# Optimization experiments

Measured on AMD Instinct MI355X. Metric: run time of the kernel, lower is better.

Reference implementation:

```python
import jax, jax.numpy as jnp
import numpy as np

B, N, D, H, K = 8, 256, 128, 128, 8


def _kaiming_uniform(key, shape, fan_in):
    bound = np.sqrt(6.0 / fan_in)
    return jax.random.uniform(key, shape, jnp.float32, -bound, bound)


def setup_inputs() -> dict:
    key = jax.random.key(0)
    ks = jax.random.split(key, 5)
    E = jax.random.normal(ks[0], (B, N, D), jnp.float32)
    W1 = _kaiming_uniform(ks[1], (K, 2 * D, H), 2 * D)   # FFN2 layer 1
    b1 = jnp.zeros((K, H), jnp.float32)
    W2 = _kaiming_uniform(ks[2], (K, H, 2), H)           # FFN2 layer 2
    b2 = jnp.zeros((K, 2), jnp.float32)
    W3 = _kaiming_uniform(ks[3], (K, 2, 1), 2)           # FFN3
    b3 = jnp.zeros((K, 1), jnp.float32)
    return {"E": E, "W1": W1, "b1": b1, "W2": W2, "b2": b2, "W3": W3, "b3": b3}


def _entmax15_pair(logits):
    # Exact alpha=1.5 entmax over a last dim of size 2 (closed form).
    # z' = z/2; p_i = [z'_i - tau]_+^2 with sum(p)=1.
    t = (logits[..., 0] - logits[..., 1]) * 0.25   # signed half-gap of z'
    d = jnp.abs(t)
    s = jnp.sqrt(jnp.maximum(0.5 - d * d, 0.0))
    p0_interior = (s + t) ** 2                      # both coords in support
    p0 = jnp.where(d >= 0.5, (t > 0).astype(logits.dtype), p0_interior)
    return jnp.stack([p0, 1.0 - p0], axis=-1)


def reference(E, W1, b1, W2, b2, W3, b3):
    # E: [B,N,D]. Concat([Ei,Ej]) @ W1 == Ei @ W1[:D] + Ej @ W1[D:], so we never
    # materialize the [B,N,N,2D] pair tensor.
    Dd = E.shape[-1]
    W1i, W1j = W1[:, :Dd, :], W1[:, Dd:, :]
    outs = []
    for h in range(W1.shape[0]):  # small fixed head loop (k_basis)
        hi = jnp.einsum('bnd,dh->bnh', E, W1i[h])
        hj = jnp.einsum('bnd,dh->bnh', E, W1j[h])
        pre = hi[:, :, None, :] + hj[:, None, :, :] + b1[h]      # [B,N,N,H]
        act = jax.nn.relu(pre)                                    # dropout: eval mode (identity)
        logits2 = jnp.einsum('bijh,hc->bijc', act, W2[h]) + b2[h]  # [B,N,N,2]
        p2 = _entmax15_pair(logits2)
        a = jnp.einsum('bijc,co->bijo', p2, W3[h])[..., 0] + b3[h][0]  # [B,N,N]
        outs.append(a)
    M = jnp.stack(outs, axis=1)  # [B,K,N,N]
    n = E.shape[1]
    eye = jnp.eye(n, dtype=M.dtype)
    M = M * (1.0 - eye)[None, None]  # no_self_loop=True
    return M
```

## Files before the change

kernel.cpp:

```cpp
#include <hip/hip_runtime.h>
#include <hip/hip_fp16.h>
#include <cstdint>
#include <cstddef>

#define B_ 8
#define N_ 256
#define D_ 128
#define H_ 128
#define K_ 8

typedef _Float16 f16x8 __attribute__((ext_vector_type(8)));
typedef _Float16 f16x2 __attribute__((ext_vector_type(2)));
typedef float    f32x4 __attribute__((ext_vector_type(4)));

static __device__ __forceinline__ f16x2 h2cast(unsigned u) {
    return __builtin_bit_cast(f16x2, u);
}
static __device__ __forceinline__ unsigned packh2(float lo, float hi) {
    unsigned a = __half_as_ushort(__float2half(lo));
    unsigned b = __half_as_ushort(__float2half(hi));
    return a | (b << 16);
}

__global__ void prep_small(const float* __restrict__ W2, const float* __restrict__ b2,
                           const float* __restrict__ W3, const float* __restrict__ b3,
                           unsigned* __restrict__ wdh, float* __restrict__ consts) {
    int t = threadIdx.x;
    for (int idx = t; idx < K_ * 64; idx += 256) {
        int base = idx * 2;
        float w0 = W2[base * 2]     - W2[base * 2 + 1];
        float w1 = W2[base * 2 + 2] - W2[base * 2 + 3];
        wdh[idx] = packh2(w0, w1);
    }
    if (t < K_) {
        consts[t * 4 + 0] = b2[t * 2] - b2[t * 2 + 1];
        consts[t * 4 + 1] = W3[t * 2] - W3[t * 2 + 1];
        consts[t * 4 + 2] = W3[t * 2 + 1] + b3[t];
    }
}

__global__ __launch_bounds__(256) void prep_eh(const float* __restrict__ E,
                                               __half* __restrict__ Eh) {
    int idx = (blockIdx.x * 256 + threadIdx.x) * 4;
    float4 v = *(const float4*)&E[idx];
    uint2 o;
    o.x = packh2(v.x, v.y);
    o.y = packh2(v.z, v.w);
    *(uint2*)&Eh[idx] = o;
}

__global__ __launch_bounds__(256) void prep_wh(const float* __restrict__ W1,
                                               __half* __restrict__ Wh) {
    __shared__ float Ws[128][33];
    const int bid = blockIdx.x;
    const int ct  = bid & 7;
    const int k   = bid >> 3;
    const int c0  = ct * 32;
    const int ro  = (c0 < 128) ? 0 : 128;
    const int h0  = c0 & 127;
    const int t   = threadIdx.x;

    #pragma unroll
    for (int rep = 0; rep < 16; rep++) {
        int idx = rep * 256 + t;
        int d   = idx >> 5;
        int cl  = idx & 31;
        Ws[d][cl] = W1[((size_t)(k * 256 + ro + d)) * H_ + h0 + cl];
    }
    __syncthreads();

    const int cl = t >> 3;
    const int dg = t & 7;
    __half tmp[16];
    #pragma unroll
    for (int e = 0; e < 16; e++) tmp[e] = __float2half(Ws[dg * 16 + e][cl]);
    *(float4*)&Wh[((size_t)(k * 256 + c0 + cl)) * D_ + dg * 16]     = *(float4*)&tmp[0];
    *(float4*)&Wh[((size_t)(k * 256 + c0 + cl)) * D_ + dg * 16 + 8] = *(float4*)&tmp[8];
}

__global__ __launch_bounds__(256) void stage1_kernel(
        const __half* __restrict__ Eh, const __half* __restrict__ Wh,
        const float* __restrict__ b1, __half* __restrict__ Gh) {
    __shared__ __half Es[64 * 136];
    __shared__ __half Ws[64 * 136];

    const int bid = blockIdx.x;
    const int ct  = bid & 3;
    const int it  = (bid >> 2) & 3;
    const int bk  = bid >> 4;
    const int k   = bk & (K_ - 1);
    const int b   = bk >> 3;
    const int i0  = it * 64, c0 = ct * 64;
    const int t   = threadIdx.x;

    #pragma unroll
    for (int rep = 0; rep < 4; rep++) {
        int idx = rep * 256 + t;
        int r = idx >> 4;
        int q = idx & 15;
        *(float4*)&Es[r * 136 + q * 8] =
            *(const float4*)&Eh[((size_t)(b * N_ + i0 + r)) * D_ + q * 8];
        *(float4*)&Ws[r * 136 + q * 8] =
            *(const float4*)&Wh[((size_t)(k * 256 + c0 + r)) * D_ + q * 8];
    }
    __syncthreads();

    const int wv   = t >> 6;
    const int lane = t & 63;
    const int wr   = wv >> 1, wc = wv & 1;
    const int lr   = lane & 15, lk = lane >> 4;

    f32x4 acc[2][2] = {{{0.f,0.f,0.f,0.f},{0.f,0.f,0.f,0.f}},
                       {{0.f,0.f,0.f,0.f},{0.f,0.f,0.f,0.f}}};
    #pragma unroll
    for (int kk = 0; kk < 4; kk++) {
        f16x8 A[2], Bv[2];
        #pragma unroll
        for (int mi = 0; mi < 2; mi++)
            A[mi] = *(const f16x8*)&Es[(wr * 32 + mi * 16 + lr) * 136 + kk * 32 + lk * 8];
        #pragma unroll
        for (int ni = 0; ni < 2; ni++)
            Bv[ni] = *(const f16x8*)&Ws[(wc * 32 + ni * 16 + lr) * 136 + kk * 32 + lk * 8];
        #pragma unroll
        for (int mi = 0; mi < 2; mi++)
            #pragma unroll
            for (int ni = 0; ni < 2; ni++)
                acc[mi][ni] = __builtin_amdgcn_mfma_f32_16x16x32_f16(
                    A[mi], Bv[ni], acc[mi][ni], 0, 0, 0);
    }

    #pragma unroll
    for (int ni = 0; ni < 2; ni++) {
        int col = c0 + wc * 32 + ni * 16 + lr;
        float bias = (col < 128) ? b1[k * H_ + col] : 0.f;
        #pragma unroll
        for (int mi = 0; mi < 2; mi++) {
            int rbase = i0 + wr * 32 + mi * 16 + lk * 4;
            #pragma unroll
            for (int r = 0; r < 4; r++) {
                Gh[((size_t)(bk * N_ + rbase + r)) * 256 + col] =
                    __float2half(acc[mi][ni][r] + bias);
            }
        }
    }
}

__global__ __launch_bounds__(256) void stage2_kernel(
        const __half* __restrict__ Gh, const unsigned* __restrict__ wdh,
        const float* __restrict__ consts, float* __restrict__ out) {
    __shared__ __half his[64 * 136];
    __shared__ __half hjs[64 * 136];

    const int bid = blockIdx.x;
    const int jt  = bid & 3;
    const int it  = (bid >> 2) & 3;
    const int bk  = bid >> 4;
    const int k   = bk & (K_ - 1);
    const int i0  = it * 64, j0 = jt * 64;
    const int t   = threadIdx.x;

    const __half* __restrict__ gb = Gh + (size_t)bk * N_ * 256;

    #pragma unroll
    for (int rep = 0; rep < 4; rep++) {
        int idx = rep * 256 + t;
        int r = idx >> 4;
        int q = idx & 15;
        *(float4*)&his[r * 136 + q * 8] =
            *(const float4*)&gb[(size_t)(i0 + r) * 256 + q * 8];
        *(float4*)&hjs[r * 136 + q * 8] =
            *(const float4*)&gb[(size_t)(j0 + r) * 256 + 128 + q * 8];
    }
    __syncthreads();

    const float b2d = consts[k * 4 + 0];
    const float w3d = consts[k * 4 + 1];
    const float w3b = consts[k * 4 + 2];
    const int tx = t & 15;
    const int ty = t >> 4;

    float acc[4][4];
    #pragma unroll
    for (int a = 0; a < 4; a++)
        #pragma unroll
        for (int c = 0; c < 4; c++) acc[a][c] = b2d;

    const unsigned* __restrict__ wp = wdh + k * 64;
    const f16x2 zz = {(_Float16)0, (_Float16)0};

    #pragma unroll 2
    for (int hq = 0; hq < 16; hq++) {
        unsigned Wv[4];
        *(uint4*)&Wv[0] = *(const uint4*)&wp[hq * 4];
        unsigned Aa[4][4], Bb[4][4];
        #pragma unroll
        for (int a = 0; a < 4; a++)
            *(uint4*)&Aa[a][0] = *(const uint4*)&his[(ty + 16 * a) * 136 + hq * 8];
        #pragma unroll
        for (int c = 0; c < 4; c++)
            *(uint4*)&Bb[c][0] = *(const uint4*)&hjs[(tx + 16 * c) * 136 + hq * 8];

        #pragma unroll
        for (int e = 0; e < 4; e++) {
            f16x2 w2 = h2cast(Wv[e]);
            #pragma unroll
            for (int a = 0; a < 4; a++) {
                f16x2 av = h2cast(Aa[a][e]);
                #pragma unroll
                for (int c = 0; c < 4; c++) {
                    f16x2 pre = av + h2cast(Bb[c][e]);
                    f16x2 act = __builtin_elementwise_max(pre, zz);
                    acc[a][c] = __builtin_amdgcn_fdot2(act, w2, acc[a][c], false);
                }
            }
        }
    }

    #pragma unroll
    for (int a = 0; a < 4; a++) {
        int i = i0 + ty + 16 * a;
        #pragma unroll
        for (int c = 0; c < 4; c++) {
            float av = acc[a][c];
            float tt = av * 0.25f;
            float dd = fabsf(tt);
            float ss = sqrtf(fmaxf(0.5f - dd * dd, 0.f));
            float p0i = (ss + tt) * (ss + tt);
            float p0 = (dd >= 0.5f) ? (tt > 0.f ? 1.f : 0.f) : p0i;
            float val = fmaf(p0, w3d, w3b);
            int j = j0 + tx + 16 * c;
            if (i == j) val = 0.f;
            out[((size_t)bk * N_ + i) * N_ + j] = val;
        }
    }
}

extern "C" void kernel_launch(void* const* d_in, const int* in_sizes, int n_in,
                              void* d_out, int out_size, void* d_ws, size_t ws_size,
                              hipStream_t stream) {
    (void)in_sizes; (void)n_in; (void)out_size; (void)ws_size;
    const float* E  = (const float*)d_in[0];
    const float* W1 = (const float*)d_in[1];
    const float* b1 = (const float*)d_in[2];
    const float* W2 = (const float*)d_in[3];
    const float* b2 = (const float*)d_in[4];
    const float* W3 = (const float*)d_in[5];
    const float* b3 = (const float*)d_in[6];
    float* out = (float*)d_out;

    char* ws = (char*)d_ws;
    unsigned* wdh   = (unsigned*)ws;
    float*    consts= (float*)(ws + 4096);
    __half*   Eh    = (__half*)(ws + 8192);
    __half*   Wh    = (__half*)(ws + 8192 + 524288);
    __half*   Gh    = (__half*)(ws + 8192 + 1048576);

    prep_small<<<1, 256, 0, stream>>>(W2, b2, W3, b3, wdh, consts);
    prep_eh<<<B_ * N_ * D_ / 1024, 256, 0, stream>>>(E, Eh);
    prep_wh<<<K_ * 8, 256, 0, stream>>>(W1, Wh);
    stage1_kernel<<<B_ * K_ * 16, 256, 0, stream>>>(Eh, Wh, b1, Gh);
    stage2_kernel<<<B_ * K_ * 16, 256, 0, stream>>>(Gh, wdh, consts, out);
}
```

Measured before the change: 58.22 us.

## Fuse projection GEMM into pairwise kernel and merge prep kernels into one launch

Merges the three prep kernels into one launch that dispatches on block index. It also removes the separate stage1 GEMM and its global Gh buffer: each pairwise block now computes its own 64-row hi and hj tiles with MFMA straight into shared memory, reading Eh and Wh fragments from global memory. This cuts two kernel launches and the Gh write/read round trip. In exchange the projection is recomputed redundantly, since each i-tile is recomputed for every j-tile and vice versa, roughly quadrupling GEMM work. It also adds a launch_bounds occupancy hint.

```diff
diff --git a/kernel.cpp b/kernel.cpp
--- a/kernel.cpp
+++ b/kernel.cpp
@@ -22,131 +22,63 @@
     return a | (b << 16);
 }
 
-__global__ void prep_small(const float* __restrict__ W2, const float* __restrict__ b2,
-                           const float* __restrict__ W3, const float* __restrict__ b3,
-                           unsigned* __restrict__ wdh, float* __restrict__ consts) {
-    int t = threadIdx.x;
-    for (int idx = t; idx < K_ * 64; idx += 256) {
-        int base = idx * 2;
-        float w0 = W2[base * 2]     - W2[base * 2 + 1];
-        float w1 = W2[base * 2 + 2] - W2[base * 2 + 3];
-        wdh[idx] = packh2(w0, w1);
-    }
-    if (t < K_) {
-        consts[t * 4 + 0] = b2[t * 2] - b2[t * 2 + 1];
-        consts[t * 4 + 1] = W3[t * 2] - W3[t * 2 + 1];
-        consts[t * 4 + 2] = W3[t * 2 + 1] + b3[t];
-    }
-}
-
-__global__ __launch_bounds__(256) void prep_eh(const float* __restrict__ E,
-                                               __half* __restrict__ Eh) {
-    int idx = (blockIdx.x * 256 + threadIdx.x) * 4;
-    float4 v = *(const float4*)&E[idx];
-    uint2 o;
-    o.x = packh2(v.x, v.y);
-    o.y = packh2(v.z, v.w);
-    *(uint2*)&Eh[idx] = o;
-}
-
-__global__ __launch_bounds__(256) void prep_wh(const float* __restrict__ W1,
-                                               __half* __restrict__ Wh) {
+__global__ __launch_bounds__(256) void prep_all(
+        const float* __restrict__ E, const float* __restrict__ W1,
+        const float* __restrict__ W2, const float* __restrict__ b2,
+        const float* __restrict__ W3, const float* __restrict__ b3,
+        __half* __restrict__ Eh, __half* __restrict__ Wh,
+        unsigned* __restrict__ wdh, float* __restrict__ consts) {
     __shared__ float Ws[128][33];
     const int bid = blockIdx.x;
-    const int ct  = bid & 7;
-    const int k   = bid >> 3;
-    const int c0  = ct * 32;
-    const int ro  = (c0 < 128) ? 0 : 128;
-    const int h0  = c0 & 127;
     const int t   = threadIdx.x;
 
-    #pragma unroll
-    for (int rep = 0; rep < 16; rep++) {
-        int idx = rep * 256 + t;
-        int d   = idx >> 5;
-        int cl  = idx & 31;
-        Ws[d][cl] = W1[((size_t)(k * 256 + ro + d)) * H_ + h0 + cl];
-    }
-    __syncthreads();
-
-    const int cl = t >> 3;
-    const int dg = t & 7;
-    __half tmp[16];
-    #pragma unroll
-    for (int e = 0; e < 16; e++) tmp[e] = __float2half(Ws[dg * 16 + e][cl]);
-    *(float4*)&Wh[((size_t)(k * 256 + c0 + cl)) * D_ + dg * 16]     = *(float4*)&tmp[0];
-    *(float4*)&Wh[((size_t)(k * 256 + c0 + cl)) * D_ + dg * 16 + 8] = *(float4*)&tmp[8];
-}
-
-__global__ __launch_bounds__(256) void stage1_kernel(
+    if (bid < 256) {
+        int idx = (bid * 256 + t) * 4;
+        float4 v = *(const float4*)&E[idx];
+        uint2 o;
+        o.x = packh2(v.x, v.y);
+        o.y = packh2(v.z, v.w);
+        *(uint2*)&Eh[idx] = o;
+    } else if (bid < 320) {
+        const int kb = bid - 256;
+        const int ct = kb & 7;
+        const int k  = kb >> 3;
+        const int c0 = ct * 32;
+        const int ro = (c0 < 128) ? 0 : 128;
+        const int h0 = c0 & 127;
+        #pragma unroll
+        for (int rep = 0; rep < 16; rep++) {
+            int idx = rep * 256 + t;
+            int d   = idx >> 5;
+            int cl  = idx & 31;
+            Ws[d][cl] = W1[((size_t)(k * 256 + ro + d)) * H_ + h0 + cl];
+        }
+        __syncthreads();
+        const int cl = t >> 3;
+        const int dg = t & 7;
+        __half tmp[16];
+        #pragma unroll
+        for (int e = 0; e < 16; e++) tmp[e] = __float2half(Ws[dg * 16 + e][cl]);
+        *(float4*)&Wh[((size_t)(k * 256 + c0 + cl)) * D_ + dg * 16]     = *(float4*)&tmp[0];
+        *(float4*)&Wh[((size_t)(k * 256 + c0 + cl)) * D_ + dg * 16 + 8] = *(float4*)&tmp[8];
+    } else {
+        for (int idx = t; idx < K_ * 64; idx += 256) {
+            int base = idx * 2;
+            float w0 = W2[base * 2]     - W2[base * 2 + 1];
+            float w1 = W2[base * 2 + 2] - W2[base * 2 + 3];
+            wdh[idx] = packh2(w0, w1);
+        }
+        if (t < K_) {
+            consts[t * 4 + 0] = b2[t * 2] - b2[t * 2 + 1];
+            consts[t * 4 + 1] = W3[t * 2] - W3[t * 2 + 1];
+            consts[t * 4 + 2] = W3[t * 2 + 1] + b3[t];
+        }
+    }
+}
+
+__global__ __launch_bounds__(256, 4) void fused_kernel(
         const __half* __restrict__ Eh, const __half* __restrict__ Wh,
-        const float* __restrict__ b1, __half* __restrict__ Gh) {
-    __shared__ __half Es[64 * 136];
-    __shared__ __half Ws[64 * 136];
-
-    const int bid = blockIdx.x;
-    const int ct  = bid & 3;
-    const int it  = (bid >> 2) & 3;
-    const int bk  = bid >> 4;
-    const int k   = bk & (K_ - 1);
-    const int b   = bk >> 3;
-    const int i0  = it * 64, c0 = ct * 64;
-    const int t   = threadIdx.x;
-
-    #pragma unroll
-    for (int rep = 0; rep < 4; rep++) {
-        int idx = rep * 256 + t;
-        int r = idx >> 4;
-        int q = idx & 15;
-        *(float4*)&Es[r * 136 + q * 8] =
-            *(const float4*)&Eh[((size_t)(b * N_ + i0 + r)) * D_ + q * 8];
-        *(float4*)&Ws[r * 136 + q * 8] =
-            *(const float4*)&Wh[((size_t)(k * 256 + c0 + r)) * D_ + q * 8];
-    }
-    __syncthreads();
-
-    const int wv   = t >> 6;
-    const int lane = t & 63;
-    const int wr   = wv >> 1, wc = wv & 1;
-    const int lr   = lane & 15, lk = lane >> 4;
-
-    f32x4 acc[2][2] = {{{0.f,0.f,0.f,0.f},{0.f,0.f,0.f,0.f}},
-                       {{0.f,0.f,0.f,0.f},{0.f,0.f,0.f,0.f}}};
-    #pragma unroll
-    for (int kk = 0; kk < 4; kk++) {
-        f16x8 A[2], Bv[2];
-        #pragma unroll
-        for (int mi = 0; mi < 2; mi++)
-            A[mi] = *(const f16x8*)&Es[(wr * 32 + mi * 16 + lr) * 136 + kk * 32 + lk * 8];
-        #pragma unroll
-        for (int ni = 0; ni < 2; ni++)
-            Bv[ni] = *(const f16x8*)&Ws[(wc * 32 + ni * 16 + lr) * 136 + kk * 32 + lk * 8];
-        #pragma unroll
-        for (int mi = 0; mi < 2; mi++)
-            #pragma unroll
-            for (int ni = 0; ni < 2; ni++)
-                acc[mi][ni] = __builtin_amdgcn_mfma_f32_16x16x32_f16(
-                    A[mi], Bv[ni], acc[mi][ni], 0, 0, 0);
-    }
-
-    #pragma unroll
-    for (int ni = 0; ni < 2; ni++) {
-        int col = c0 + wc * 32 + ni * 16 + lr;
-        float bias = (col < 128) ? b1[k * H_ + col] : 0.f;
-        #pragma unroll
-        for (int mi = 0; mi < 2; mi++) {
-            int rbase = i0 + wr * 32 + mi * 16 + lk * 4;
-            #pragma unroll
-            for (int r = 0; r < 4; r++) {
-                Gh[((size_t)(bk * N_ + rbase + r)) * 256 + col] =
-                    __float2half(acc[mi][ni][r] + bias);
-            }
-        }
-    }
-}
-
-__global__ __launch_bounds__(256) void stage2_kernel(
-        const __half* __restrict__ Gh, const unsigned* __restrict__ wdh,
+        const float* __restrict__ b1, const unsigned* __restrict__ wdh,
         const float* __restrict__ consts, float* __restrict__ out) {
     __shared__ __half his[64 * 136];
     __shared__ __half hjs[64 * 136];
@@ -156,20 +88,49 @@
     const int it  = (bid >> 2) & 3;
     const int bk  = bid >> 4;
     const int k   = bk & (K_ - 1);
+    const int b   = bk >> 3;
     const int i0  = it * 64, j0 = jt * 64;
     const int t   = threadIdx.x;
-
-    const __half* __restrict__ gb = Gh + (size_t)bk * N_ * 256;
-
-    #pragma unroll
-    for (int rep = 0; rep < 4; rep++) {
-        int idx = rep * 256 + t;
-        int r = idx >> 4;
-        int q = idx & 15;
-        *(float4*)&his[r * 136 + q * 8] =
-            *(const float4*)&gb[(size_t)(i0 + r) * 256 + q * 8];
-        *(float4*)&hjs[r * 136 + q * 8] =
-            *(const float4*)&gb[(size_t)(j0 + r) * 256 + 128 + q * 8];
+    const int wv   = t >> 6;
+    const int lane = t & 63;
+    const int lr   = lane & 15, lk = lane >> 4;
+
+    {
+        const bool isJ   = (wv >= 2);
+        const int  half32 = wv & 1;
+        const int  rowbase = (isJ ? j0 : i0) + half32 * 32;
+        const int  cbase   = isJ ? 128 : 0;
+        __half* __restrict__ dst = isJ ? hjs : his;
+
+        f16x8 A[2][4];
+        #pragma unroll
+        for (int mi = 0; mi < 2; mi++)
+            #pragma unroll
+            for (int kk = 0; kk < 4; kk++)
+                A[mi][kk] = *(const f16x8*)&Eh[
+                    ((size_t)(b * N_ + rowbase + mi * 16 + lr)) * D_ + kk * 32 + lk * 8];
+
+        #pragma unroll
+        for (int nc = 0; nc < 8; nc++) {
+            f16x8 Bf[4];
+            #pragma unroll
+            for (int kk = 0; kk < 4; kk++)
+                Bf[kk] = *(const f16x8*)&Wh[
+                    ((size_t)(k * 256 + cbase + nc * 16 + lr)) * D_ + kk * 32 + lk * 8];
+            const int hcol = nc * 16 + lr;
+            const float bias = isJ ? 0.f : b1[k * H_ + hcol];
+            #pragma unroll
+            for (int mi = 0; mi < 2; mi++) {
+                f32x4 acc = {0.f, 0.f, 0.f, 0.f};
+                #pragma unroll
+                for (int kk = 0; kk < 4; kk++)
+                    acc = __builtin_amdgcn_mfma_f32_16x16x32_f16(A[mi][kk], Bf[kk], acc, 0, 0, 0);
+                const int lrow = half32 * 32 + mi * 16 + lk * 4;
+                #pragma unroll
+                for (int q = 0; q < 4; q++)
+                    dst[(lrow + q) * 136 + hcol] = __float2half(acc[q] + bias);
+            }
+        }
     }
     __syncthreads();
 
@@ -249,15 +210,11 @@
     float* out = (float*)d_out;
 
     char* ws = (char*)d_ws;
-    unsigned* wdh   = (unsigned*)ws;
-    float*    consts= (float*)(ws + 4096);
-    __half*   Eh    = (__half*)(ws + 8192);
-    __half*   Wh    = (__half*)(ws + 8192 + 524288);
-    __half*   Gh    = (__half*)(ws + 8192 + 1048576);
-
-    prep_small<<<1, 256, 0, stream>>>(W2, b2, W3, b3, wdh, consts);
-    prep_eh<<<B_ * N_ * D_ / 1024, 256, 0, stream>>>(E, Eh);
-    prep_wh<<<K_ * 8, 256, 0, stream>>>(W1, Wh);
-    stage1_kernel<<<B_ * K_ * 16, 256, 0, stream>>>(Eh, Wh, b1, Gh);
-    stage2_kernel<<<B_ * K_ * 16, 256, 0, stream>>>(Gh, wdh, consts, out);
-}
+    unsigned* wdh    = (unsigned*)ws;
+    float*    consts = (float*)(ws + 4096);
+    __half*   Eh     = (__half*)(ws + 8192);
+    __half*   Wh     = (__half*)(ws + 8192 + 524288);
+
+    prep_all<<<321, 256, 0, stream>>>(E, W1, W2, b2, W3, b3, Eh, Wh, wdh, consts);
+    fused_kernel<<<B_ * K_ * 16, 256, 0, stream>>>(Eh, Wh, b1, wdh, consts, out);
+}
```

Result: faster. 56.16 us (-3.5%).
